# Kernel tuning notes

Hardware: AMD Instinct MI355X
Metric: run time of the kernel (lower is better)

The kernel has to match this reference:

```python
import jax, jax.numpy as jnp
import numpy as np

MAX_DEG = 10
MIN_DEG = 0
N_FEAT = 128
NB_FILTER = 128
BATCH = 128
DEG_COUNT = 30000                      # atoms per degree bucket (static)
N_ATOMS = (MAX_DEG + 1) * DEG_COUNT    # 330000, atoms sorted by degree (deg0 first)
NB_AFFINE = 3 * MAX_DEG + (2 - MIN_DEG)  # 32
EPS = 1e-5


def setup_inputs() -> dict:
    key = jax.random.key(0)
    ks = jax.random.split(key, 16)
    atoms = jax.random.normal(ks[0], (N_ATOMS, N_FEAT), dtype=jnp.float32)
    membership = jax.random.randint(ks[1], (N_ATOMS,), 0, BATCH)
    # deg_slice[d] = [start, count] for degree d (atoms sorted by degree)
    deg_slice = jnp.stack([jnp.arange(MAX_DEG + 1) * DEG_COUNT,
                           jnp.full((MAX_DEG + 1,), DEG_COUNT)], axis=1)
    inp = {"atoms": atoms, "deg_slice": deg_slice, "membership": membership}
    for d in range(1, MAX_DEG + 1):
        inp[f"adj{d}"] = jax.random.randint(ks[1 + d], (DEG_COUNT, d), 0, N_ATOMS)
    glorot = (2.0 / (N_FEAT + NB_FILTER)) ** 0.5
    inp["W"] = jax.random.normal(ks[12], (NB_AFFINE, N_FEAT, NB_FILTER), dtype=jnp.float32) * glorot
    inp["b"] = jnp.zeros((NB_AFFINE, NB_FILTER), dtype=jnp.float32)
    inp["gamma"] = jnp.ones((NB_FILTER,), dtype=jnp.float32)
    inp["beta"] = jnp.zeros((NB_FILTER,), dtype=jnp.float32)
    return inp


def _self_slice(atoms, deg):
    return jax.lax.dynamic_slice_in_dim(atoms, deg * DEG_COUNT, DEG_COUNT, axis=0)


def _norm(x, gamma, beta):
    m = jnp.mean(x, axis=-1, keepdims=True)
    std = jnp.sqrt(jnp.var(x, axis=-1, keepdims=True) + EPS)
    return gamma * ((x - m) / (std + EPS)) + beta


def _forward(atoms, W, b, gamma, beta, membership, adjs):
    # W consumption order matches the TF iterator: for deg=1..max_deg -> (rel, self),
    # then deg0 self at index 2*MAX_DEG, then gather affines deg1..max_deg, deg0 last.
    rel_outs = [None] * (MAX_DEG + 1)
    gather_outs = [None] * (MAX_DEG + 1)
    for d in range(1, MAX_DEG + 1):
        neigh = jnp.sum(atoms[adjs[d - 1]], axis=1)          # (COUNT, F) gather+sum
        self_a = _self_slice(atoms, d)                        # (COUNT, F)
        i_rel, i_self = 2 * (d - 1), 2 * d - 1
        rel_outs[d] = (neigh @ W[i_rel] + b[i_rel]) + (self_a @ W[i_self] + b[i_self])
        i_g = 2 * MAX_DEG + d
        gather_outs[d] = self_a @ W[i_g] + b[i_g]
    self0 = _self_slice(atoms, 0)
    rel_outs[0] = self0 @ W[2 * MAX_DEG] + b[2 * MAX_DEG]
    gather_outs[0] = self0 @ W[NB_AFFINE - 1] + b[NB_AFFINE - 1]

    activated = jnp.concatenate(rel_outs, axis=0)             # (N_ATOMS, NB_FILTER)
    gathered = jnp.concatenate(gather_outs, axis=0)           # (N_ATOMS, NB_FILTER)
    # graph_gather: per-molecule sum (dynamic_partition + reduce_sum)
    atom_gather = jax.ops.segment_sum(gathered, membership, num_segments=BATCH)

    xn = _norm(activated, gamma, beta)                        # per-row "BN" as in source
    yn = _norm(atom_gather, gamma, beta)
    # gather_node: per-molecule max of normalized atom features
    g = jax.ops.segment_max(xn, membership, num_segments=BATCH)
    return xn, yn, g


def reference(atoms, deg_slice, membership, adj1, adj2, adj3, adj4, adj5,
              adj6, adj7, adj8, adj9, adj10, W, b, gamma, beta):
    adjs = (adj1, adj2, adj3, adj4, adj5, adj6, adj7, adj8, adj9, adj10)
    return _forward(atoms, W, b, gamma, beta, membership, adjs)
```

## Files before the change

kernel.cpp:

```cpp
#include <hip/hip_runtime.h>
#include <stdint.h>

#define MAX_DEG   10
#define DEG_COUNT 30000
#define N_ATOMS   330000
#define NF        128
#define BATCH     128
#define SORT_BLOCKS 256
#define SORT_CHUNK  1290
#define NB_BUILD  1408
#define NB_CAST   41250

typedef __attribute__((ext_vector_type(8))) short bf16x8;
typedef __attribute__((ext_vector_type(4))) float f32x4;
typedef __attribute__((ext_vector_type(2))) float f32x2;

__device__ __forceinline__ float bf2f(unsigned short h) {
  union { unsigned u; float f; } v; v.u = ((unsigned)h) << 16; return v.f;
}
__device__ __forceinline__ unsigned short f2bf(float f) {
  union { float f; unsigned u; } v; v.f = f;
  unsigned u = v.u;
  unsigned r = (u + 0x7fffu + ((u >> 16) & 1u)) >> 16;
  return (unsigned short)r;
}

struct AdjPtrs { const int* p[10]; };

#define NEG_INF_BITS 0xFF800000

__global__ __launch_bounds__(256) void k_prep(
    const float* __restrict__ W,
    const float* __restrict__ b,
    const f32x4* __restrict__ atoms4,
    const int* __restrict__ membership,
    unsigned short* __restrict__ BcatT,
    float* __restrict__ biascat,
    ushort4* __restrict__ dst4,
    int* __restrict__ blockHistT)
{
  const int bx = blockIdx.x;
  const int tid = threadIdx.x;
  __shared__ int bins[BATCH];

  if (bx < NB_BUILD) {
    int idx = bx * 256 + tid;
    if (idx < 11 * 128) {
      int d = idx >> 7, n = idx & 127;
      float f = (d >= 1) ? (b[(2 * (d - 1)) * 128 + n] + b[(2 * d - 1) * 128 + n])
                         : b[20 * 128 + n];
      biascat[idx] = f;
    }
    if (idx < 11 * 128 * 256) {
      int d = idx >> 15;
      int rem = idx & 32767;
      int n = rem >> 8;
      int k = rem & 255;
      float v;
      if (k < 128) {
        v = (d >= 1) ? W[(2 * (d - 1)) * 16384 + k * 128 + n] : 0.f;
      } else {
        int ks = k - 128;
        int wi = (d >= 1) ? (2 * d - 1) : 20;
        v = W[wi * 16384 + ks * 128 + n];
      }
      BcatT[idx] = f2bf(v);
    }
  } else if (bx < NB_BUILD + NB_CAST) {
    size_t i = (size_t)(bx - NB_BUILD) * 256 + tid;
    f32x4 v = __builtin_nontemporal_load(atoms4 + i);
    ushort4 o;
    o.x = f2bf(v[0]); o.y = f2bf(v[1]); o.z = f2bf(v[2]); o.w = f2bf(v[3]);
    dst4[i] = o;
  } else {
    int bh = bx - NB_BUILD - NB_CAST;
    if (tid < BATCH) bins[tid] = 0;
    __syncthreads();
    int lo = bh * SORT_CHUNK, hi = min(lo + SORT_CHUNK, N_ATOMS);
    for (int i = lo + tid; i < hi; i += 256)
      atomicAdd(&bins[membership[i]], 1);
    __syncthreads();
    if (tid < BATCH) blockHistT[tid * 256 + bh] = bins[tid];
  }
}

__global__ __launch_bounds__(256) void k_scan(
    const int* __restrict__ blockHistT,
    int* __restrict__ relOffT,
    int* __restrict__ tot)
{
  const int m = blockIdx.x;
  const int tid = threadIdx.x;
  __shared__ int ws[4];
  int v = blockHistT[m * 256 + tid];
  int x = v;
#pragma unroll
  for (int o = 1; o < 64; o <<= 1) {
    int t = __shfl_up(x, o, 64);
    if ((tid & 63) >= o) x += t;
  }
  if ((tid & 63) == 63) ws[tid >> 6] = x;
  __syncthreads();
  int wb = 0;
  for (int w = 0; w < (tid >> 6); ++w) wb += ws[w];
  int incl = wb + x;
  relOffT[m * 256 + tid] = incl - v;
  if (tid == 255) tot[m] = incl;
}

__global__ __launch_bounds__(256) void k_scatter(
    const int* __restrict__ membership,
    const int* __restrict__ relOffT,
    const int* __restrict__ tot,
    int* __restrict__ perm)
{
  __shared__ int totS[BATCH], baseS[BATCH], bins[BATCH];
  const int tid = threadIdx.x;
  if (tid < BATCH) totS[tid] = tot[tid];
  __syncthreads();
  if (tid == 0) {
    int a = 0;
    for (int i = 0; i < BATCH; ++i) { baseS[i] = a; a += totS[i]; }
  }
  __syncthreads();
  if (tid < BATCH) bins[tid] = baseS[tid] + relOffT[tid * 256 + blockIdx.x];
  __syncthreads();
  int lo = blockIdx.x * SORT_CHUNK, hi = min(lo + SORT_CHUNK, N_ATOMS);
  for (int i = lo + tid; i < hi; i += 256) {
    int m = membership[i];
    int pos = atomicAdd(&bins[m], 1);
    perm[pos] = i;
  }
}

template<int D>
__device__ __forceinline__ void nsum_phase0(const unsigned* __restrict__ atomsU,
                                            const int* __restrict__ abase,
                                            unsigned* __restrict__ NS,
                                            int rowTile, int wave, int lane) {
  for (int it = 0; it < 8; ++it) {
    int iloc = wave * 16 + it * 2;
    int r0 = rowTile * 128 + iloc;
    int sw0 = lane ^ ((iloc & 7) << 2);
    int sw1 = lane ^ (((iloc + 1) & 7) << 2);
    if (r0 < DEG_COUNT - 1) {
      const int* a = abase + (size_t)r0 * D;
      int myIdx = (lane < 2 * D) ? a[lane] : 0;
      unsigned xs[2 * D];
#pragma unroll
      for (int j = 0; j < 2 * D; ++j) {
        int nbr = __shfl(myIdx, j, 64);
        xs[j] = atomsU[(size_t)nbr * 64 + lane];
      }
      float s0a = 0.f, s1a = 0.f, s0b = 0.f, s1b = 0.f;
#pragma unroll
      for (int j = 0; j < D; ++j) {
        s0a += bf2f((unsigned short)(xs[j] & 0xffff));
        s1a += bf2f((unsigned short)(xs[j] >> 16));
      }
#pragma unroll
      for (int j = D; j < 2 * D; ++j) {
        s0b += bf2f((unsigned short)(xs[j] & 0xffff));
        s1b += bf2f((unsigned short)(xs[j] >> 16));
      }
      NS[(size_t)iloc * 64 + sw0]       = (unsigned)f2bf(s0a) | ((unsigned)f2bf(s1a) << 16);
      NS[(size_t)(iloc + 1) * 64 + sw1] = (unsigned)f2bf(s0b) | ((unsigned)f2bf(s1b) << 16);
    } else {
      const int* a = abase + (size_t)(DEG_COUNT - 1) * D;
      int myIdx = (lane < D) ? a[lane] : 0;
      unsigned xs[D];
#pragma unroll
      for (int j = 0; j < D; ++j) {
        int nbr = __shfl(myIdx, j, 64);
        xs[j] = atomsU[(size_t)nbr * 64 + lane];
      }
      float s0 = 0.f, s1 = 0.f;
#pragma unroll
      for (int j = 0; j < D; ++j) {
        s0 += bf2f((unsigned short)(xs[j] & 0xffff));
        s1 += bf2f((unsigned short)(xs[j] >> 16));
      }
      unsigned p = (unsigned)f2bf(s0) | ((unsigned)f2bf(s1) << 16);
      NS[(size_t)iloc * 64 + sw0] = p;
      NS[(size_t)(iloc + 1) * 64 + sw1] = p;
    }
  }
}

__global__ __launch_bounds__(512, 4) void k_gemm(
    const unsigned short* __restrict__ atomsBf,
    AdjPtrs adj,
    const unsigned short* __restrict__ BcatT,
    const float* __restrict__ biascat,
    const float* __restrict__ gamma,
    const float* __restrict__ beta,
    float* __restrict__ out0)
{
  const int d = blockIdx.y;
  const int rowTile = blockIdx.x;
  const int tid = threadIdx.x;
  const int lane = tid & 63;
  const int wave = tid >> 6;
  const int m16 = lane & 15;
  const int g = lane >> 4;

  __shared__ unsigned short Bs[128 * 256];
  unsigned* NS = (unsigned*)Bs;

  const unsigned short* Bd = BcatT + d * 32768;
  const unsigned* atomsU = (const unsigned*)atomsBf;

  const int rowBase = rowTile * 128 + wave * 16;
  bf16x8 af[8];
  {
    int rbL = rowBase + m16; if (rbL > DEG_COUNT - 1) rbL = DEG_COUNT - 1;
    size_t gr = (size_t)d * DEG_COUNT + rbL;
#pragma unroll
    for (int ks = 4; ks < 8; ++ks)
      af[ks] = *(const bf16x8*)(atomsBf + gr * 128 + (ks - 4) * 32 + g * 8);
  }

  if (d > 0) {
    const int* abase = adj.p[d - 1];
    switch (d) {
      case 1:  nsum_phase0<1>(atomsU, abase, NS, rowTile, wave, lane); break;
      case 2:  nsum_phase0<2>(atomsU, abase, NS, rowTile, wave, lane); break;
      case 3:  nsum_phase0<3>(atomsU, abase, NS, rowTile, wave, lane); break;
      case 4:  nsum_phase0<4>(atomsU, abase, NS, rowTile, wave, lane); break;
      case 5:  nsum_phase0<5>(atomsU, abase, NS, rowTile, wave, lane); break;
      case 6:  nsum_phase0<6>(atomsU, abase, NS, rowTile, wave, lane); break;
      case 7:  nsum_phase0<7>(atomsU, abase, NS, rowTile, wave, lane); break;
      case 8:  nsum_phase0<8>(atomsU, abase, NS, rowTile, wave, lane); break;
      case 9:  nsum_phase0<9>(atomsU, abase, NS, rowTile, wave, lane); break;
      default: nsum_phase0<10>(atomsU, abase, NS, rowTile, wave, lane); break;
    }
    __syncthreads();
    const char* nsb = (const char*)NS;
    const int rowb = (wave * 16 + m16) * 256;
    const int sw = (m16 & 7) << 4;
#pragma unroll
    for (int ks = 0; ks < 4; ++ks)
      af[ks] = *(const bf16x8*)(nsb + ((rowb + ks * 64 + g * 16) ^ sw));
    __syncthreads();
  } else {
    bf16x8 z = {0, 0, 0, 0, 0, 0, 0, 0};
#pragma unroll
    for (int ks = 0; ks < 4; ++ks) af[ks] = z;
  }

#pragma unroll
  for (int it = 0; it < 8; ++it) {
    int flat = it * 512 + tid;
    int row = flat >> 5;
    int c = flat & 31;
    uint4 v = *(const uint4*)(Bd + row * 256 + c * 8);
    int kb = (c * 16) ^ ((row & 7) << 4);
    *(uint4*)((char*)Bs + row * 512 + kb) = v;
  }

  __syncthreads();

  const int ldsMask = (m16 & 7) << 4;

  f32x4 acc[8];
#pragma unroll
  for (int ct = 0; ct < 8; ++ct) acc[ct] = (f32x4){0.f, 0.f, 0.f, 0.f};

#pragma unroll
  for (int ct = 0; ct < 8; ++ct) {
    const char* bbase = (const char*)Bs + (ct * 16 + m16) * 512;
    bf16x8 bf[8];
#pragma unroll
    for (int ks = 0; ks < 8; ++ks)
      bf[ks] = *(const bf16x8*)(bbase + ((ks * 64 + g * 16) ^ ldsMask));
#pragma unroll
    for (int ks = 0; ks < 8; ++ks)
      acc[ct] = __builtin_amdgcn_mfma_f32_16x16x32_bf16(af[ks], bf[ks], acc[ct], 0, 0, 0);
  }

  float bias_[8], gam[8], bet[8];
#pragma unroll
  for (int ct = 0; ct < 8; ++ct) {
    bias_[ct] = biascat[d * 128 + ct * 16 + m16];
    gam[ct] = gamma[ct * 16 + m16];
    bet[ct] = beta[ct * 16 + m16];
  }

#pragma unroll
  for (int ct = 0; ct < 8; ++ct)
#pragma unroll
    for (int r = 0; r < 4; ++r) acc[ct][r] += bias_[ct];

  float s[4], qq[4];
#pragma unroll
  for (int r = 0; r < 4; ++r) {
    s[r] = 0.f; qq[r] = 0.f;
#pragma unroll
    for (int ct = 0; ct < 8; ++ct) {
      float v = acc[ct][r];
      s[r] += v; qq[r] += v * v;
    }
  }
#pragma unroll
  for (int off = 8; off >= 1; off >>= 1) {
#pragma unroll
    for (int r = 0; r < 4; ++r) {
      s[r]  += __shfl_xor(s[r],  off, 64);
      qq[r] += __shfl_xor(qq[r], off, 64);
    }
  }

#pragma unroll
  for (int r = 0; r < 4; ++r) {
    int rb = rowBase + g * 4 + r;
    float mean = s[r] * (1.0f / 128.0f);
    float var  = qq[r] * (1.0f / 128.0f) - mean * mean;
    float inv  = 1.0f / (sqrtf(var + 1e-5f) + 1e-5f);
    if (rb < DEG_COUNT) {
      size_t grow = (size_t)d * DEG_COUNT + rb;
#pragma unroll
      for (int ct = 0; ct < 8; ++ct)
        out0[grow * 128 + ct * 16 + m16] = gam[ct] * ((acc[ct][r] - mean) * inv) + bet[ct];
    }
  }
}

__global__ __launch_bounds__(512) void k_mreduce(
    const f32x2* __restrict__ xnV,
    const unsigned* __restrict__ atomsU,
    const int* __restrict__ perm,
    const int* __restrict__ tot,
    float* __restrict__ Spart,
    int* __restrict__ cntPart,
    float2* __restrict__ pmax4)
{
  const int m = blockIdx.x >> 2;
  const int s = blockIdx.x & 3;
  const int wave = threadIdx.x >> 6, lane = threadIdx.x & 63;

  __shared__ float S[8][11][128];
  __shared__ int C[8][11];
  __shared__ float2 maxT[8][64];
  __shared__ int totS[BATCH];
  __shared__ int rangeS[2];
  for (int e = lane; e < 11 * 128; e += 64) S[wave][e >> 7][e & 127] = 0.f;
  if (lane < 11) C[wave][lane] = 0;
  if (threadIdx.x < BATCH) totS[threadIdx.x] = tot[threadIdx.x];
  __syncthreads();
  if (threadIdx.x == 0) {
    int a = 0;
    for (int i = 0; i < m; ++i) a += totS[i];
    rangeS[0] = a; rangeS[1] = totS[m];
  }
  __syncthreads();
  const int b0 = rangeS[0], cnt = rangeS[1];
  const int lo = b0 + (cnt * s) / 4;
  const int hi = b0 + (cnt * (s + 1)) / 4;

  const float NEG_INF = __int_as_float((int)NEG_INF_BITS);
  float mx0 = NEG_INF, mx1 = NEG_INF;

  for (int i = lo + wave * 2; i < hi; i += 16) {
    int r0 = perm[i];
    bool has1 = (i + 1 < hi);
    int r1 = has1 ? perm[i + 1] : r0;
    f32x2 x0 = __builtin_nontemporal_load(xnV + (size_t)r0 * 64 + lane);
    unsigned a0 = __builtin_nontemporal_load(atomsU + (size_t)r0 * 64 + lane);
    f32x2 x1 = __builtin_nontemporal_load(xnV + (size_t)r1 * 64 + lane);
    unsigned a1 = __builtin_nontemporal_load(atomsU + (size_t)r1 * 64 + lane);
    int d0 = r0 / DEG_COUNT;
    mx0 = fmaxf(mx0, x0[0]);
    mx1 = fmaxf(mx1, x0[1]);
    S[wave][d0][lane]      += bf2f((unsigned short)(a0 & 0xffff));
    S[wave][d0][64 + lane] += bf2f((unsigned short)(a0 >> 16));
    if (lane == 0) C[wave][d0]++;
    if (has1) {
      int d1 = r1 / DEG_COUNT;
      mx0 = fmaxf(mx0, x1[0]);
      mx1 = fmaxf(mx1, x1[1]);
      S[wave][d1][lane]      += bf2f((unsigned short)(a1 & 0xffff));
      S[wave][d1][64 + lane] += bf2f((unsigned short)(a1 >> 16));
      if (lane == 0) C[wave][d1]++;
    }
  }
  maxT[wave][lane] = make_float2(mx0, mx1);
  __syncthreads();

  if (threadIdx.x < 64) {
    int l = threadIdx.x;
    float2 mm = maxT[0][l];
#pragma unroll
    for (int w = 1; w < 8; ++w) {
      float2 b = maxT[w][l]; mm.x = fmaxf(mm.x, b.x); mm.y = fmaxf(mm.y, b.y);
    }
    pmax4[(s * 128 + m) * 64 + l] = mm;
  }
  for (int e = threadIdx.x; e < 11 * 128; e += 512) {
    int d = e >> 7, p = e & 127;
    float t = 0.f;
#pragma unroll
    for (int w = 0; w < 8; ++w) t += S[w][d][p];
    int col = (p < 64) ? (2 * p) : (2 * (p - 64) + 1);
    Spart[(((size_t)s * 128 + m) * 11 + d) * 128 + col] = t;
  }
  if (threadIdx.x < 11) {
    int t = 0;
#pragma unroll
    for (int w = 0; w < 8; ++w) t += C[w][threadIdx.x];
    cntPart[((size_t)s * 128 + m) * 11 + threadIdx.x] = t;
  }
}

__global__ __launch_bounds__(128) void k_ynfinal(
    const float* __restrict__ Spart,
    const int* __restrict__ cntPart,
    const float* __restrict__ W,
    const float* __restrict__ b,
    const float* __restrict__ gamma,
    const float* __restrict__ beta,
    const float* __restrict__ pmax4,
    float* __restrict__ out1,
    float* __restrict__ out2)
{
  int m = blockIdx.x;
  int j = threadIdx.x;

  float g = __int_as_float((int)NEG_INF_BITS);
#pragma unroll
  for (int sl = 0; sl < 4; ++sl)
    g = fmaxf(g, pmax4[(sl * 128 + m) * 128 + j]);
  out2[m * 128 + j] = g;

  __shared__ float Sm[11][128];
  __shared__ float cw[11];
  for (int e = j; e < 11 * 128; e += 128) {
    int d = e >> 7, c = e & 127;
    float t = 0.f;
#pragma unroll
    for (int sl = 0; sl < 4; ++sl)
      t += Spart[(((size_t)sl * 128 + m) * 11 + d) * 128 + c];
    Sm[d][c] = t;
  }
  if (j < 11) {
    int t = 0;
#pragma unroll
    for (int sl = 0; sl < 4; ++sl) t += cntPart[((size_t)sl * 128 + m) * 11 + j];
    cw[j] = (float)t;
  }
  __syncthreads();

  float acc = 0.f;
  for (int d = 0; d < 11; ++d) {
    int wi = (d >= 1) ? (20 + d) : 31;
    const float* Wd = W + wi * 16384;
    float a0 = 0.f, a1 = 0.f, a2 = 0.f, a3 = 0.f;
    for (int k = 0; k < 128; k += 4) {
      a0 += Sm[d][k]     * Wd[k * 128 + j];
      a1 += Sm[d][k + 1] * Wd[(k + 1) * 128 + j];
      a2 += Sm[d][k + 2] * Wd[(k + 2) * 128 + j];
      a3 += Sm[d][k + 3] * Wd[(k + 3) * 128 + j];
    }
    acc += (a0 + a1) + (a2 + a3);
    acc += cw[d] * b[wi * 128 + j];
  }

  float ws_ = acc, wq = acc * acc;
#pragma unroll
  for (int off = 32; off >= 1; off >>= 1) {
    ws_ += __shfl_xor(ws_, off, 64);
    wq  += __shfl_xor(wq, off, 64);
  }
  __shared__ float red[4];
  int wave = j >> 6, lane = j & 63;
  if (lane == 0) { red[wave * 2] = ws_; red[wave * 2 + 1] = wq; }
  __syncthreads();
  float Ssum = red[0] + red[2], Q = red[1] + red[3];
  float mean = Ssum * (1.f / 128.f);
  float var = Q * (1.f / 128.f) - mean * mean;
  float inv = 1.f / (sqrtf(var + 1e-5f) + 1e-5f);
  out1[m * 128 + j] = gamma[j] * ((acc - mean) * inv) + beta[j];
}

extern "C" void kernel_launch(void* const* d_in, const int* in_sizes, int n_in,
                              void* d_out, int out_size, void* d_ws, size_t ws_size,
                              hipStream_t stream) {
  const float* atoms = (const float*)d_in[0];
  const int* membership = (const int*)d_in[2];
  AdjPtrs adj;
  for (int i = 0; i < 10; ++i) adj.p[i] = (const int*)d_in[3 + i];
  const float* W     = (const float*)d_in[13];
  const float* b     = (const float*)d_in[14];
  const float* gamma = (const float*)d_in[15];
  const float* beta  = (const float*)d_in[16];

  char* ws = (char*)d_ws;
  size_t off = 0;
  unsigned short* atomsBf = (unsigned short*)(ws + off); off += (size_t)N_ATOMS * 128 * 2;
  unsigned short* BcatT   = (unsigned short*)(ws + off); off += (size_t)11 * 128 * 256 * 2;
  float* biascat          = (float*)(ws + off);          off += (size_t)11 * 128 * 4;
  int* perm               = (int*)(ws + off);            off += (size_t)N_ATOMS * 4;
  int* tot                = (int*)(ws + off);            off += 512;
  int* blockHistT         = (int*)(ws + off);            off += (size_t)BATCH * SORT_BLOCKS * 4;
  int* relOffT            = (int*)(ws + off);            off += (size_t)BATCH * SORT_BLOCKS * 4;
  float* Spart            = (float*)(ws + off);          off += (size_t)4 * 128 * 11 * 128 * 4;
  int* cntPart            = (int*)(ws + off);            off += (size_t)4 * 128 * 11 * 4;
  float* pmax4            = (float*)(ws + off);          off += (size_t)4 * 128 * 128 * 4;

  float* out0 = (float*)d_out;
  float* out1 = out0 + (size_t)N_ATOMS * 128;
  float* out2 = out1 + 16384;

  hipLaunchKernelGGL(k_prep, dim3(NB_BUILD + NB_CAST + SORT_BLOCKS), dim3(256), 0, stream,
                     W, b, (const f32x4*)atoms, membership,
                     BcatT, biascat, (ushort4*)atomsBf, blockHistT);
  hipLaunchKernelGGL(k_scan, dim3(128), dim3(256), 0, stream, blockHistT, relOffT, tot);
  hipLaunchKernelGGL(k_scatter, dim3(SORT_BLOCKS), dim3(256), 0, stream,
                     membership, relOffT, tot, perm);
  hipLaunchKernelGGL(k_gemm, dim3(236, 11), dim3(512), 0, stream,
                     atomsBf, adj, BcatT, biascat, gamma, beta, out0);
  hipLaunchKernelGGL(k_mreduce, dim3(512), dim3(512), 0, stream,
                     (const f32x2*)out0, (const unsigned*)atomsBf, perm, tot,
                     Spart, cntPart, (float2*)pmax4);
  hipLaunchKernelGGL(k_ynfinal, dim3(128), dim3(128), 0, stream,
                     Spart, cntPart, W, b, gamma, beta, pmax4, out1, out2);
}
```

Before: 498.5 us.

## Halve GEMM LDS by staging B in two K-halves; split molecule reduce into eight slices

```diff
diff --git a/kernel.cpp b/kernel.cpp
--- a/kernel.cpp
+++ b/kernel.cpp
@@ -10,6 +10,7 @@
 #define SORT_CHUNK  1290
 #define NB_BUILD  1408
 #define NB_CAST   41250
+#define NSLICES   8
 
 typedef __attribute__((ext_vector_type(8))) short bf16x8;
 typedef __attribute__((ext_vector_type(4))) float f32x4;
@@ -204,7 +205,7 @@
   const int m16 = lane & 15;
   const int g = lane >> 4;
 
-  __shared__ unsigned short Bs[128 * 256];
+  __shared__ unsigned short Bs[128 * 128];
   unsigned* NS = (unsigned*)Bs;
 
   const unsigned short* Bd = BcatT + d * 32768;
@@ -241,41 +242,42 @@
 #pragma unroll
     for (int ks = 0; ks < 4; ++ks)
       af[ks] = *(const bf16x8*)(nsb + ((rowb + ks * 64 + g * 16) ^ sw));
-    __syncthreads();
   } else {
     bf16x8 z = {0, 0, 0, 0, 0, 0, 0, 0};
 #pragma unroll
     for (int ks = 0; ks < 4; ++ks) af[ks] = z;
   }
 
-#pragma unroll
-  for (int it = 0; it < 8; ++it) {
-    int flat = it * 512 + tid;
-    int row = flat >> 5;
-    int c = flat & 31;
-    uint4 v = *(const uint4*)(Bd + row * 256 + c * 8);
-    int kb = (c * 16) ^ ((row & 7) << 4);
-    *(uint4*)((char*)Bs + row * 512 + kb) = v;
-  }
-
-  __syncthreads();
+  f32x4 acc[8];
+#pragma unroll
+  for (int ct = 0; ct < 8; ++ct) acc[ct] = (f32x4){0.f, 0.f, 0.f, 0.f};
 
   const int ldsMask = (m16 & 7) << 4;
 
-  f32x4 acc[8];
-#pragma unroll
-  for (int ct = 0; ct < 8; ++ct) acc[ct] = (f32x4){0.f, 0.f, 0.f, 0.f};
-
-#pragma unroll
-  for (int ct = 0; ct < 8; ++ct) {
-    const char* bbase = (const char*)Bs + (ct * 16 + m16) * 512;
-    bf16x8 bf[8];
-#pragma unroll
-    for (int ks = 0; ks < 8; ++ks)
-      bf[ks] = *(const bf16x8*)(bbase + ((ks * 64 + g * 16) ^ ldsMask));
-#pragma unroll
-    for (int ks = 0; ks < 8; ++ks)
-      acc[ct] = __builtin_amdgcn_mfma_f32_16x16x32_bf16(af[ks], bf[ks], acc[ct], 0, 0, 0);
+#pragma unroll
+  for (int h = 0; h < 2; ++h) {
+    __syncthreads();
+#pragma unroll
+    for (int it = 0; it < 4; ++it) {
+      int flat = it * 512 + tid;
+      int row = flat >> 4;
+      int c = flat & 15;
+      uint4 v = *(const uint4*)(Bd + row * 256 + h * 128 + c * 8);
+      int kb = (c * 16) ^ ((row & 7) << 4);
+      *(uint4*)((char*)Bs + row * 256 + kb) = v;
+    }
+    __syncthreads();
+#pragma unroll
+    for (int ct = 0; ct < 8; ++ct) {
+      const char* bbase = (const char*)Bs + (ct * 16 + m16) * 256;
+      bf16x8 bf[4];
+#pragma unroll
+      for (int ks = 0; ks < 4; ++ks)
+        bf[ks] = *(const bf16x8*)(bbase + ((ks * 64 + g * 16) ^ ldsMask));
+#pragma unroll
+      for (int ks = 0; ks < 4; ++ks)
+        acc[ct] = __builtin_amdgcn_mfma_f32_16x16x32_bf16(af[h * 4 + ks], bf[ks], acc[ct], 0, 0, 0);
+    }
   }
 
   float bias_[8], gam[8], bet[8];
@@ -334,8 +336,8 @@
     int* __restrict__ cntPart,
     float2* __restrict__ pmax4)
 {
-  const int m = blockIdx.x >> 2;
-  const int s = blockIdx.x & 3;
+  const int m = blockIdx.x >> 3;
+  const int s = blockIdx.x & 7;
   const int wave = threadIdx.x >> 6, lane = threadIdx.x & 63;
 
   __shared__ float S[8][11][128];
@@ -354,8 +356,8 @@
   }
   __syncthreads();
   const int b0 = rangeS[0], cnt = rangeS[1];
-  const int lo = b0 + (cnt * s) / 4;
-  const int hi = b0 + (cnt * (s + 1)) / 4;
+  const int lo = b0 + (cnt * s) / NSLICES;
+  const int hi = b0 + (cnt * (s + 1)) / NSLICES;
 
   const float NEG_INF = __int_as_float((int)NEG_INF_BITS);
   float mx0 = NEG_INF, mx1 = NEG_INF;
@@ -393,7 +395,7 @@
     for (int w = 1; w < 8; ++w) {
       float2 b = maxT[w][l]; mm.x = fmaxf(mm.x, b.x); mm.y = fmaxf(mm.y, b.y);
     }
-    pmax4[(s * 128 + m) * 64 + l] = mm;
+    pmax4[((size_t)s * 128 + m) * 64 + l] = mm;
   }
   for (int e = threadIdx.x; e < 11 * 128; e += 512) {
     int d = e >> 7, p = e & 127;
@@ -427,8 +429,8 @@
 
   float g = __int_as_float((int)NEG_INF_BITS);
 #pragma unroll
-  for (int sl = 0; sl < 4; ++sl)
-    g = fmaxf(g, pmax4[(sl * 128 + m) * 128 + j]);
+  for (int sl = 0; sl < NSLICES; ++sl)
+    g = fmaxf(g, pmax4[((size_t)sl * 128 + m) * 128 + j]);
   out2[m * 128 + j] = g;
 
   __shared__ float Sm[11][128];
@@ -437,14 +439,15 @@
     int d = e >> 7, c = e & 127;
     float t = 0.f;
 #pragma unroll
-    for (int sl = 0; sl < 4; ++sl)
+    for (int sl = 0; sl < NSLICES; ++sl)
       t += Spart[(((size_t)sl * 128 + m) * 11 + d) * 128 + c];
     Sm[d][c] = t;
   }
   if (j < 11) {
     int t = 0;
 #pragma unroll
-    for (int sl = 0; sl < 4; ++sl) t += cntPart[((size_t)sl * 128 + m) * 11 + j];
+    for (int sl = 0; sl < NSLICES; ++sl)
+      t += cntPart[((size_t)sl * 128 + m) * 11 + j];
     cw[j] = (float)t;
   }
   __syncthreads();
@@ -502,9 +505,9 @@
   int* tot                = (int*)(ws + off);            off += 512;
   int* blockHistT         = (int*)(ws + off);            off += (size_t)BATCH * SORT_BLOCKS * 4;
   int* relOffT            = (int*)(ws + off);            off += (size_t)BATCH * SORT_BLOCKS * 4;
-  float* Spart            = (float*)(ws + off);          off += (size_t)4 * 128 * 11 * 128 * 4;
-  int* cntPart            = (int*)(ws + off);            off += (size_t)4 * 128 * 11 * 4;
-  float* pmax4            = (float*)(ws + off);          off += (size_t)4 * 128 * 128 * 4;
+  float* Spart            = (float*)(ws + off);          off += (size_t)NSLICES * 128 * 11 * 128 * 4;
+  int* cntPart            = (int*)(ws + off);            off += (size_t)NSLICES * 128 * 11 * 4;
+  float* pmax4            = (float*)(ws + off);          off += (size_t)NSLICES * 128 * 128 * 4;
 
   float* out0 = (float*)d_out;
   float* out1 = out0 + (size_t)N_ATOMS * 128;
@@ -518,7 +521,7 @@
                      membership, relOffT, tot, perm);
   hipLaunchKernelGGL(k_gemm, dim3(236, 11), dim3(512), 0, stream,
                      atomsBf, adj, BcatT, biascat, gamma, beta, out0);
-  hipLaunchKernelGGL(k_mreduce, dim3(512), dim3(512), 0, stream,
+  hipLaunchKernelGGL(k_mreduce, dim3(128 * NSLICES), dim3(512), 0, stream,
                      (const f32x2*)out0, (const unsigned*)atomsBf, perm, tot,
                      Spart, cntPart, (float2*)pmax4);
   hipLaunchKernelGGL(k_ynfinal, dim3(128), dim3(128), 0, stream,
```

Result: slower. 508.8 us (+2.1%).
